# Kernel optimization log

Hardware: AMD Instinct MI355X
Metric: run time of the kernel (lower is better)

## Reference

```python
import jax, jax.numpy as jnp
import numpy as np

B, S, E, H = 4, 1024, 2048, 16
D = E // H  # head_dim = 128


def setup_inputs() -> dict:
    key = jax.random.key(0)
    k1, k2, k3, k4, k5 = jax.random.split(key, 5)
    scale = 1.0 / np.sqrt(E)
    return {
        "query": jax.random.normal(k1, (B, S, E), dtype=jnp.float32),
        "in_proj_weight": jax.random.normal(k2, (3 * E, E), dtype=jnp.float32) * scale,
        "in_proj_bias": jax.random.normal(k3, (3 * E,), dtype=jnp.float32) * 0.02,
        "out_proj_weight": jax.random.normal(k4, (E, E), dtype=jnp.float32) * scale,
        "out_proj_bias": jax.random.normal(k5, (E,), dtype=jnp.float32) * 0.02,
    }


def reference(query, in_proj_weight, in_proj_bias, out_proj_weight, out_proj_bias):
    b, s, e = query.shape
    d = e // H
    # fused QKV projection: [B,S,3E]
    proj = jnp.einsum("bse,fe->bsf", query, in_proj_weight) + in_proj_bias
    q, k, v = jnp.split(proj, 3, axis=-1)
    # [B,S,E] -> [B,H,S,D]
    def to_heads(t):
        return t.reshape(b, s, H, d).transpose(0, 2, 1, 3)
    q, k, v = to_heads(q), to_heads(k), to_heads(v)
    # scaled dot-product attention (non-causal, no mask, no dropout)
    scores = jnp.einsum("bhqd,bhkd->bhqk", q, k) / jnp.sqrt(jnp.asarray(d, q.dtype))
    attn = jax.nn.softmax(scores, axis=-1)
    ctx = jnp.einsum("bhqk,bhkd->bhqd", attn, v)
    # [B,H,S,D] -> [B,S,E]
    ctx = ctx.transpose(0, 2, 1, 3).reshape(b, s, e)
    out = jnp.einsum("bse,fe->bsf", ctx, out_proj_weight) + out_proj_bias
    return out
```

## Files before the change

### kernel.cpp

```cpp
#include <hip/hip_runtime.h>
#include <hip/hip_fp16.h>

#define F16 _Float16
typedef F16 f16x8 __attribute__((ext_vector_type(8)));
typedef F16 f16x4 __attribute__((ext_vector_type(4)));
typedef float f32x4 __attribute__((ext_vector_type(4)));

__global__ void cvt_f32_f16(const float* __restrict__ src, F16* __restrict__ dst, int n) {
    int idx = blockIdx.x * blockDim.x + threadIdx.x;
    int stride = gridDim.x * blockDim.x;
    for (int i = idx * 4; i < n; i += stride * 4) {
        float4 v = *reinterpret_cast<const float4*>(src + i);
        f16x4 o;
        o[0] = (F16)v.x; o[1] = (F16)v.y; o[2] = (F16)v.z; o[3] = (F16)v.w;
        *reinterpret_cast<f16x4*>(dst + i) = o;
    }
}

__device__ __forceinline__ void gl_lds16(const F16* g, F16* l) {
    __builtin_amdgcn_global_load_lds(
        (const __attribute__((address_space(1))) void*)g,
        (__attribute__((address_space(3))) void*)l, 16, 0, 0);
}

__global__ __launch_bounds__(512, 2) void gemm8qkv(
    const F16* __restrict__ A, const F16* __restrict__ Bw, const float* __restrict__ bias,
    F16* __restrict__ q_ws, F16* __restrict__ k_ws, F16* __restrict__ v_ws,
    int M, int N, int K)
{
    __shared__ __align__(16) F16 lds[2][4][8192];
    const int tid = threadIdx.x;
    const int w = tid >> 6, l = tid & 63;
    const int lr = l & 15, lg = l >> 4;
    const int wm = w >> 2, wn = w & 3;

    const int xcd = (int)blockIdx.x & 7, s5 = (int)blockIdx.x >> 3;
    const int mb = (xcd & 1) * 8 + s5 / 6;
    const int nb = (xcd >> 1) * 6 + s5 % 6;
    const long brow = (long)mb * 256, bcol = (long)nb * 256;

    const F16* rb0 = A + brow * K;
    const F16* rb1 = rb0 + 128 * (long)K;
    const F16* rb2 = Bw + bcol * K;
    const F16* rb3 = rb2 + 128 * (long)K;

    const int sr0 = ((tid >> 7) << 4) + (tid & 15);
    const int skk = (((tid >> 6) & 1) << 5) + (((tid >> 4) & 3) << 3);
    const int wb8 = (w << 6) * 8;

#define GISSUE(BUF, R, S, KT, RB) \
    gl_lds16(RB + (long)(sr0 + S * 64) * K + (KT) * 64 + skk, \
             &lds[BUF][R][S * 4096 + wb8])

    const int NK = K >> 6;

    f32x4 acc[8][4];
#pragma unroll
    for (int f = 0; f < 8; ++f)
#pragma unroll
        for (int nf = 0; nf < 4; ++nf) acc[f][nf] = f32x4{0.f, 0.f, 0.f, 0.f};

    GISSUE(0, 0, 0, 0, rb0); GISSUE(0, 0, 1, 0, rb0);
    GISSUE(0, 1, 0, 0, rb1); GISSUE(0, 1, 1, 0, rb1);
    GISSUE(0, 2, 0, 0, rb2); GISSUE(0, 2, 1, 0, rb2);
    GISSUE(0, 3, 0, 0, rb3); GISSUE(0, 3, 1, 0, rb3);
    if (NK > 1) {
        GISSUE(1, 2, 0, 1, rb2); GISSUE(1, 2, 1, 1, rb2);
        GISSUE(1, 3, 0, 1, rb3); GISSUE(1, 3, 1, 1, rb3);
        GISSUE(1, 0, 0, 1, rb0); GISSUE(1, 1, 0, 1, rb1);
        asm volatile("s_waitcnt vmcnt(6)" ::: "memory");
    } else {
        asm volatile("s_waitcnt vmcnt(0)" ::: "memory");
    }
    __builtin_amdgcn_s_barrier();

    for (int kt = 0; kt < NK; ++kt) {
        const int cur = kt & 1, nxt = cur ^ 1;
        const F16* Areg = &lds[cur][wm][0];
        const F16* Breg = &lds[cur][2 + (wn >> 1)][0];
        f16x8 b[4][2];
#pragma unroll
        for (int nf = 0; nf < 4; ++nf)
#pragma unroll
            for (int ks = 0; ks < 2; ++ks)
                b[nf][ks] = *reinterpret_cast<const f16x8*>(
                    Breg + ((((wn & 1) * 4 + nf) * 2 + ks) * 64 + l) * 8);
#pragma unroll
        for (int p = 0; p < 4; ++p) {
            f16x8 a[2][2];
#pragma unroll
            for (int mf = 0; mf < 2; ++mf)
#pragma unroll
                for (int ks = 0; ks < 2; ++ks)
                    a[mf][ks] = *reinterpret_cast<const f16x8*>(
                        Areg + (((2 * p + mf) * 2 + ks) * 64 + l) * 8);
            if (p == 0) {
                if (kt + 1 < NK) { GISSUE(nxt, 0, 1, kt + 1, rb0); GISSUE(nxt, 1, 1, kt + 1, rb1); }
            } else if (p == 1) {
                if (kt + 2 < NK) { GISSUE(cur, 2, 0, kt + 2, rb2); GISSUE(cur, 2, 1, kt + 2, rb2); }
            } else if (p == 2) {
                if (kt + 2 < NK) { GISSUE(cur, 3, 0, kt + 2, rb3); GISSUE(cur, 3, 1, kt + 2, rb3); }
            } else {
                if (kt + 2 < NK) { GISSUE(cur, 0, 0, kt + 2, rb0); GISSUE(cur, 1, 0, kt + 2, rb1); }
            }
            __builtin_amdgcn_sched_barrier(0);
            __builtin_amdgcn_s_barrier();
            asm volatile("s_waitcnt lgkmcnt(0)" ::: "memory");
            __builtin_amdgcn_sched_barrier(0);
            __builtin_amdgcn_s_setprio(1);
#pragma unroll
            for (int mf = 0; mf < 2; ++mf)
#pragma unroll
                for (int nf = 0; nf < 4; ++nf)
#pragma unroll
                    for (int ks = 0; ks < 2; ++ks)
                        acc[2 * p + mf][nf] = __builtin_amdgcn_mfma_f32_16x16x32_f16(
                            a[mf][ks], b[nf][ks], acc[2 * p + mf][nf], 0, 0, 0);
            __builtin_amdgcn_s_setprio(0);
            __builtin_amdgcn_sched_barrier(0);
            if (p == 3) {
                if (kt + 2 < NK) asm volatile("s_waitcnt vmcnt(6)" ::: "memory");
                else             asm volatile("s_waitcnt vmcnt(0)" ::: "memory");
            }
            __builtin_amdgcn_s_barrier();
        }
    }
#undef GISSUE

    const int col0 = (int)bcol + wn * 64;
    const int row0 = (int)brow + wm * 128;
    const int part = (int)(bcol >> 11);
    const int bI = row0 >> 10;
    const int sb = row0 & 1023;
    const float scl = (part == 0) ? 0.08838834764831845f : 1.0f;
#pragma unroll
    for (int nf = 0; nf < 4; ++nf) {
        const int gcol = col0 + nf * 16 + lr;
        const float bv = bias[gcol];
        const int d = gcol & 127;
        const int hh = (gcol >> 7) & 15;
        if (part == 2) {
            F16* dst0 = v_ws + ((long)((bI * 16 + hh) * 128 + d)) * 1024;
#pragma unroll
            for (int f = 0; f < 8; ++f) {
                f16x4 pv;
#pragma unroll
                for (int r = 0; r < 4; ++r) pv[r] = (F16)(acc[f][nf][r] + bv);
                *reinterpret_cast<f16x4*>(dst0 + sb + f * 16 + lg * 4) = pv;
            }
        } else {
            F16* dst0 = ((part == 0) ? q_ws : k_ws) + ((long)(bI * 16 + hh) * 1024) * 128 + d;
#pragma unroll
            for (int f = 0; f < 8; ++f)
#pragma unroll
                for (int r = 0; r < 4; ++r)
                    dst0[(long)(sb + f * 16 + lg * 4 + r) * 128] =
                        (F16)((acc[f][nf][r] + bv) * scl);
        }
    }
}

__global__ __launch_bounds__(512, 2) void gemm8out(
    const F16* __restrict__ A, const F16* __restrict__ Bw, const float* __restrict__ bias,
    float* __restrict__ fout, int M, int N, int K)
{
    __shared__ __align__(16) F16 lds[2][3][8192];
    const int tid = threadIdx.x;
    const int w = tid >> 6, l = tid & 63;
    const int lr = l & 15, lg = l >> 4;
    const int wm = w >> 2, wn = w & 3;

    const int xcd = (int)blockIdx.x & 7, s5 = (int)blockIdx.x >> 3;
    const int mb = (xcd & 3) * 8 + (s5 >> 2);
    const int nb = (xcd >> 2) * 4 + (s5 & 3);
    const long brow = (long)mb * 128, bcol = (long)nb * 256;

    const F16* rbA = A + brow * K;
    const F16* rb2 = Bw + bcol * K;
    const F16* rb3 = rb2 + 128 * (long)K;

    const int sr0 = ((tid >> 7) << 4) + (tid & 15);
    const int skk = (((tid >> 6) & 1) << 5) + (((tid >> 4) & 3) << 3);
    const int wb8 = (w << 6) * 8;

#define GISSUE(BUF, R, S, KT, RB) \
    gl_lds16(RB + (long)(sr0 + S * 64) * K + (KT) * 64 + skk, \
             &lds[BUF][R][S * 4096 + wb8])

    const int NK = K >> 6;

    f32x4 acc[4][4];
#pragma unroll
    for (int f = 0; f < 4; ++f)
#pragma unroll
        for (int nf = 0; nf < 4; ++nf) acc[f][nf] = f32x4{0.f, 0.f, 0.f, 0.f};

    GISSUE(0, 0, 0, 0, rbA); GISSUE(0, 0, 1, 0, rbA);
    GISSUE(0, 1, 0, 0, rb2); GISSUE(0, 1, 1, 0, rb2);
    GISSUE(0, 2, 0, 0, rb3); GISSUE(0, 2, 1, 0, rb3);
    if (NK > 1) {
        GISSUE(1, 1, 0, 1, rb2); GISSUE(1, 1, 1, 1, rb2);
        GISSUE(1, 2, 0, 1, rb3); GISSUE(1, 2, 1, 1, rb3);
        asm volatile("s_waitcnt vmcnt(4)" ::: "memory");
    } else {
        asm volatile("s_waitcnt vmcnt(0)" ::: "memory");
    }
    __builtin_amdgcn_s_barrier();

    for (int kt = 0; kt < NK; ++kt) {
        const int cur = kt & 1, nxt = cur ^ 1;
        const F16* Areg = &lds[cur][0][0];
        const F16* Breg = &lds[cur][1 + (wn >> 1)][0];
        f16x8 b[4][2];
#pragma unroll
        for (int nf = 0; nf < 4; ++nf)
#pragma unroll
            for (int ks = 0; ks < 2; ++ks)
                b[nf][ks] = *reinterpret_cast<const f16x8*>(
                    Breg + ((((wn & 1) * 4 + nf) * 2 + ks) * 64 + l) * 8);
#pragma unroll
        for (int p = 0; p < 2; ++p) {
            f16x8 a[2][2];
#pragma unroll
            for (int mf = 0; mf < 2; ++mf)
#pragma unroll
                for (int ks = 0; ks < 2; ++ks)
                    a[mf][ks] = *reinterpret_cast<const f16x8*>(
                        Areg + (((wm * 4 + 2 * p + mf) * 2 + ks) * 64 + l) * 8);
            if (p == 0) {
                if (kt + 1 < NK) { GISSUE(nxt, 0, 0, kt + 1, rbA); GISSUE(nxt, 0, 1, kt + 1, rbA); }
            } else {
                if (kt + 2 < NK) {
                    GISSUE(cur, 1, 0, kt + 2, rb2); GISSUE(cur, 1, 1, kt + 2, rb2);
                    GISSUE(cur, 2, 0, kt + 2, rb3); GISSUE(cur, 2, 1, kt + 2, rb3);
                }
            }
            __builtin_amdgcn_sched_barrier(0);
            __builtin_amdgcn_s_barrier();
            asm volatile("s_waitcnt lgkmcnt(0)" ::: "memory");
            __builtin_amdgcn_sched_barrier(0);
            __builtin_amdgcn_s_setprio(1);
#pragma unroll
            for (int mf = 0; mf < 2; ++mf)
#pragma unroll
                for (int nf = 0; nf < 4; ++nf)
#pragma unroll
                    for (int ks = 0; ks < 2; ++ks)
                        acc[2 * p + mf][nf] = __builtin_amdgcn_mfma_f32_16x16x32_f16(
                            a[mf][ks], b[nf][ks], acc[2 * p + mf][nf], 0, 0, 0);
            __builtin_amdgcn_s_setprio(0);
            __builtin_amdgcn_sched_barrier(0);
            if (p == 1) {
                if (kt + 2 < NK) asm volatile("s_waitcnt vmcnt(4)" ::: "memory");
                else             asm volatile("s_waitcnt vmcnt(0)" ::: "memory");
            }
            __builtin_amdgcn_s_barrier();
        }
    }
#undef GISSUE

    const int col0 = (int)bcol + wn * 64;
    const int row0 = (int)brow + wm * 64;
#pragma unroll
    for (int nf = 0; nf < 4; ++nf) {
        const int gcol = col0 + nf * 16 + lr;
        const float bv = bias[gcol];
#pragma unroll
        for (int f = 0; f < 4; ++f)
#pragma unroll
            for (int r = 0; r < 4; ++r)
                fout[(long)(row0 + f * 16 + lg * 4 + r) * N + gcol] = acc[f][nf][r] + bv;
    }
}

__global__ __launch_bounds__(256, 2) void attn_kernel(
    const F16* __restrict__ q_ws, const F16* __restrict__ k_ws,
    const F16* __restrict__ v_ws, F16* __restrict__ ctx)
{
    __shared__ __align__(16) F16 kt[2][64 * 128];
    __shared__ __align__(16) F16 vt[2][128 * 64];
    __shared__ __align__(16) F16 p_lds[4][2048];
    const int tid = threadIdx.x;
    const int w = tid >> 6, l = tid & 63;
    const int lr = l & 15, lg = l >> 4;
    const int work = (blockIdx.x & 7) * 64 + (blockIdx.x >> 3);
    const int bh = work >> 3, qt = work & 7;
    const int b = bh >> 4, h = bh & 15;
    const int q0 = qt * 128 + w * 32;

    const F16* kbh = k_ws + (long)bh * 1024 * 128;
    const F16* vbh = v_ws + (long)bh * 128 * 1024;

    f16x8 qf[2][4];
#pragma unroll
    for (int mi = 0; mi < 2; ++mi)
#pragma unroll
        for (int ks = 0; ks < 4; ++ks)
            qf[mi][ks] = *reinterpret_cast<const f16x8*>(
                q_ws + ((long)bh * 1024 + q0 + mi * 16 + lr) * 128 + ks * 32 + lg * 8);

    auto stage = [&](int buf, int kv0) {
#pragma unroll
        for (int t = 0; t < 4; ++t) {
            const int chunk = t * 256 + tid;
            const int row = chunk >> 4;
            const int colb = (chunk & 15) << 4;
            const int gcol = colb ^ ((row & 7) << 4);
            gl_lds16(kbh + (long)(kv0 + row) * 128 + (gcol >> 1),
                     &kt[buf][(t * 256 + w * 64) * 8]);
        }
#pragma unroll
        for (int t = 0; t < 4; ++t) {
            const int chunk = t * 256 + tid;
            const int d = chunk >> 3;
            const int colb = (chunk & 7) << 4;
            const int gcol = colb ^ ((d & 7) << 4);
            gl_lds16(vbh + (long)d * 1024 + kv0 + (gcol >> 1),
                     &vt[buf][(t * 256 + w * 64) * 8]);
        }
    };

    float mrun[2][4], lsum[2][4];
#pragma unroll
    for (int mi = 0; mi < 2; ++mi)
#pragma unroll
        for (int r = 0; r < 4; ++r) { mrun[mi][r] = -1e30f; lsum[mi][r] = 0.f; }
    f32x4 acc[2][8];
#pragma unroll
    for (int mi = 0; mi < 2; ++mi)
#pragma unroll
        for (int nf = 0; nf < 8; ++nf) acc[mi][nf] = f32x4{0.f, 0.f, 0.f, 0.f};

    stage(0, 0);
    __syncthreads();
    int cur = 0;
    for (int it = 0; it < 16; ++it) {
        if (it + 1 < 16) stage(cur ^ 1, (it + 1) * 64);

        f32x4 sc[2][4];
#pragma unroll
        for (int mi = 0; mi < 2; ++mi)
#pragma unroll
            for (int cf = 0; cf < 4; ++cf) sc[mi][cf] = f32x4{0.f, 0.f, 0.f, 0.f};
#pragma unroll
        for (int cf = 0; cf < 4; ++cf) {
#pragma unroll
            for (int ks = 0; ks < 4; ++ks) {
                const int row = cf * 16 + lr;
                const int eff = (ks * 64 + lg * 16) ^ ((row & 7) << 4);
                f16x8 kf = *reinterpret_cast<const f16x8*>(&kt[cur][row * 128 + (eff >> 1)]);
#pragma unroll
                for (int mi = 0; mi < 2; ++mi)
                    sc[mi][cf] = __builtin_amdgcn_mfma_f32_16x16x32_f16(qf[mi][ks], kf, sc[mi][cf], 0, 0, 0);
            }
        }

#pragma unroll
        for (int mi = 0; mi < 2; ++mi) {
            float t4[4];
#pragma unroll
            for (int r = 0; r < 4; ++r)
                t4[r] = fmaxf(fmaxf(sc[mi][0][r], sc[mi][1][r]), fmaxf(sc[mi][2][r], sc[mi][3][r]));
#pragma unroll
            for (int msk = 1; msk < 16; msk <<= 1)
#pragma unroll
                for (int r = 0; r < 4; ++r) t4[r] = fmaxf(t4[r], __shfl_xor(t4[r], msk));
            float al[4], rs[4], p[4][4];
#pragma unroll
            for (int r = 0; r < 4; ++r) {
                const float mn = fmaxf(mrun[mi][r], t4[r]);
                al[r] = __expf(mrun[mi][r] - mn);
                mrun[mi][r] = mn;
#pragma unroll
                for (int cf = 0; cf < 4; ++cf) p[cf][r] = __expf(sc[mi][cf][r] - mn);
                rs[r] = (p[0][r] + p[1][r]) + (p[2][r] + p[3][r]);
            }
#pragma unroll
            for (int msk = 1; msk < 16; msk <<= 1)
#pragma unroll
                for (int r = 0; r < 4; ++r) rs[r] += __shfl_xor(rs[r], msk);
#pragma unroll
            for (int r = 0; r < 4; ++r) lsum[mi][r] = lsum[mi][r] * al[r] + rs[r];
#pragma unroll
            for (int nf = 0; nf < 8; ++nf)
#pragma unroll
                for (int r = 0; r < 4; ++r) acc[mi][nf][r] *= al[r];
#pragma unroll
            for (int cf = 0; cf < 4; ++cf)
#pragma unroll
                for (int r = 0; r < 4; ++r) {
                    const int chunk = (mi * 2 + (cf >> 1)) * 64 + (lg * 4 + r) + ((cf & 1) * 2 + (lr >> 3)) * 16;
                    p_lds[w][chunk * 8 + (lr & 7)] = (F16)p[cf][r];
                }
        }

        f16x8 pf[2][2];
#pragma unroll
        for (int mi = 0; mi < 2; ++mi)
#pragma unroll
            for (int half = 0; half < 2; ++half)
                pf[mi][half] = *reinterpret_cast<const f16x8*>(&p_lds[w][((mi * 2 + half) * 64 + l) * 8]);
#pragma unroll
        for (int nf = 0; nf < 8; ++nf) {
#pragma unroll
            for (int half = 0; half < 2; ++half) {
                const int d = nf * 16 + lr;
                const int eff = (half * 64 + lg * 16) ^ ((d & 7) << 4);
                f16x8 vf = *reinterpret_cast<const f16x8*>(&vt[cur][d * 64 + (eff >> 1)]);
#pragma unroll
                for (int mi = 0; mi < 2; ++mi)
                    acc[mi][nf] = __builtin_amdgcn_mfma_f32_16x16x32_f16(pf[mi][half], vf, acc[mi][nf], 0, 0, 0);
            }
        }
        __syncthreads();
        cur ^= 1;
    }

#pragma unroll
    for (int mi = 0; mi < 2; ++mi) {
        float inv[4];
#pragma unroll
        for (int r = 0; r < 4; ++r) inv[r] = 1.f / lsum[mi][r];
#pragma unroll
        for (int nf = 0; nf < 8; ++nf)
#pragma unroll
            for (int r = 0; r < 4; ++r) {
                const int s = q0 + mi * 16 + lg * 4 + r;
                const int e = h * 128 + nf * 16 + lr;
                ctx[((long)(b * 1024 + s)) * 2048 + e] = (F16)(acc[mi][nf][r] * inv[r]);
            }
    }
}

extern "C" void kernel_launch(void* const* d_in, const int* in_sizes, int n_in,
                              void* d_out, int out_size, void* d_ws, size_t ws_size,
                              hipStream_t stream) {
    const float* query = (const float*)d_in[0];
    const float* w_in  = (const float*)d_in[1];
    const float* b_in  = (const float*)d_in[2];
    const float* w_out = (const float*)d_in[3];
    const float* b_out = (const float*)d_in[4];
    float* out = (float*)d_out;

    char* ws = (char*)d_ws;
    size_t off = 0;
    auto carve = [&](size_t bytes) -> void* {
        void* p = ws + off;
        off += (bytes + 255) & ~(size_t)255;
        return p;
    };
    F16* xq  = (F16*)carve(8388608ULL * 2);
    F16* wih = (F16*)carve(12582912ULL * 2);
    F16* woh = (F16*)carve(4194304ULL * 2);
    F16* qws = (F16*)carve(8388608ULL * 2);
    F16* kws = (F16*)carve(8388608ULL * 2);
    F16* vws = (F16*)carve(8388608ULL * 2);
    F16* ctx = (F16*)carve(8388608ULL * 2);

    cvt_f32_f16<<<1024, 256, 0, stream>>>(query, xq, 8388608);
    cvt_f32_f16<<<1024, 256, 0, stream>>>(w_in, wih, 12582912);
    cvt_f32_f16<<<512, 256, 0, stream>>>(w_out, woh, 4194304);

    gemm8qkv<<<384, 512, 0, stream>>>(xq, wih, b_in, qws, kws, vws, 4096, 6144, 2048);
    attn_kernel<<<512, 256, 0, stream>>>(qws, kws, vws, ctx);
    gemm8out<<<256, 512, 0, stream>>>(ctx, woh, b_out, out, 4096, 2048, 2048);
}
```

Measured before the change: 402.8 us.

## Transpose attention MFMA operands and add lazy softmax rescaling

Swaps the MFMA A/B operands in both QK^T and PV so each lane holds one query row. Row max and sum then need only two cross-lane shuffles instead of four, and P is written to LDS as swizzled f16x4 vectors. A wave-uniform threshold skips updating the running max and rescaling the accumulator when the new max exceeds the old by no more than 8. That trades a bounded exp growth in fp32 for fewer multiplies. The output store becomes vectorized f16x4 per row.

```diff
diff --git a/kernel.cpp b/kernel.cpp
--- a/kernel.cpp
+++ b/kernel.cpp
@@ -279,7 +279,7 @@
 {
     __shared__ __align__(16) F16 kt[2][64 * 128];
     __shared__ __align__(16) F16 vt[2][128 * 64];
-    __shared__ __align__(16) F16 p_lds[4][2048];
+    __shared__ __align__(16) F16 plds[4][2][1024];
     const int tid = threadIdx.x;
     const int w = tid >> 6, l = tid & 63;
     const int lr = l & 15, lg = l >> 4;
@@ -287,6 +287,7 @@
     const int bh = work >> 3, qt = work & 7;
     const int b = bh >> 4, h = bh & 15;
     const int q0 = qt * 128 + w * 32;
+    const int sw = (lr & 7) << 4;
 
     const F16* kbh = k_ws + (long)bh * 1024 * 128;
     const F16* vbh = v_ws + (long)bh * 128 * 1024;
@@ -320,11 +321,9 @@
         }
     };
 
-    float mrun[2][4], lsum[2][4];
-#pragma unroll
-    for (int mi = 0; mi < 2; ++mi)
-#pragma unroll
-        for (int r = 0; r < 4; ++r) { mrun[mi][r] = -1e30f; lsum[mi][r] = 0.f; }
+    float mrun[2], lsum[2];
+    mrun[0] = mrun[1] = -1e30f;
+    lsum[0] = lsum[1] = 0.f;
     f32x4 acc[2][8];
 #pragma unroll
     for (int mi = 0; mi < 2; ++mi)
@@ -351,65 +350,64 @@
                 f16x8 kf = *reinterpret_cast<const f16x8*>(&kt[cur][row * 128 + (eff >> 1)]);
 #pragma unroll
                 for (int mi = 0; mi < 2; ++mi)
-                    sc[mi][cf] = __builtin_amdgcn_mfma_f32_16x16x32_f16(qf[mi][ks], kf, sc[mi][cf], 0, 0, 0);
+                    sc[mi][cf] = __builtin_amdgcn_mfma_f32_16x16x32_f16(kf, qf[mi][ks], sc[mi][cf], 0, 0, 0);
             }
         }
 
 #pragma unroll
         for (int mi = 0; mi < 2; ++mi) {
-            float t4[4];
-#pragma unroll
-            for (int r = 0; r < 4; ++r)
-                t4[r] = fmaxf(fmaxf(sc[mi][0][r], sc[mi][1][r]), fmaxf(sc[mi][2][r], sc[mi][3][r]));
-#pragma unroll
-            for (int msk = 1; msk < 16; msk <<= 1)
-#pragma unroll
-                for (int r = 0; r < 4; ++r) t4[r] = fmaxf(t4[r], __shfl_xor(t4[r], msk));
-            float al[4], rs[4], p[4][4];
-#pragma unroll
-            for (int r = 0; r < 4; ++r) {
-                const float mn = fmaxf(mrun[mi][r], t4[r]);
-                al[r] = __expf(mrun[mi][r] - mn);
-                mrun[mi][r] = mn;
-#pragma unroll
-                for (int cf = 0; cf < 4; ++cf) p[cf][r] = __expf(sc[mi][cf][r] - mn);
-                rs[r] = (p[0][r] + p[1][r]) + (p[2][r] + p[3][r]);
-            }
-#pragma unroll
-            for (int msk = 1; msk < 16; msk <<= 1)
-#pragma unroll
-                for (int r = 0; r < 4; ++r) rs[r] += __shfl_xor(rs[r], msk);
-#pragma unroll
-            for (int r = 0; r < 4; ++r) lsum[mi][r] = lsum[mi][r] * al[r] + rs[r];
-#pragma unroll
-            for (int nf = 0; nf < 8; ++nf)
-#pragma unroll
-                for (int r = 0; r < 4; ++r) acc[mi][nf][r] *= al[r];
+            float nm = sc[mi][0][0];
 #pragma unroll
             for (int cf = 0; cf < 4; ++cf)
 #pragma unroll
+                for (int r = 0; r < 4; ++r) nm = fmaxf(nm, sc[mi][cf][r]);
+            nm = fmaxf(nm, __shfl_xor(nm, 16));
+            nm = fmaxf(nm, __shfl_xor(nm, 32));
+            const bool skip = __all(nm <= mrun[mi] + 8.0f);
+            float mn, al;
+            if (skip) { mn = mrun[mi]; al = 1.0f; }
+            else      { mn = fmaxf(mrun[mi], nm); al = __expf(mrun[mi] - mn); mrun[mi] = mn; }
+            float rs = 0.f;
+            char* prow = reinterpret_cast<char*>(&plds[w][mi][0]) + lr * 128;
+#pragma unroll
+            for (int cf = 0; cf < 4; ++cf) {
+                f16x4 pv;
+#pragma unroll
                 for (int r = 0; r < 4; ++r) {
-                    const int chunk = (mi * 2 + (cf >> 1)) * 64 + (lg * 4 + r) + ((cf & 1) * 2 + (lr >> 3)) * 16;
-                    p_lds[w][chunk * 8 + (lr & 7)] = (F16)p[cf][r];
+                    const float pe = __expf(sc[mi][cf][r] - mn);
+                    rs += pe;
+                    pv[r] = (F16)pe;
                 }
+                *reinterpret_cast<f16x4*>(prow + ((cf * 32 + lg * 8) ^ sw)) = pv;
+            }
+            rs += __shfl_xor(rs, 16);
+            rs += __shfl_xor(rs, 32);
+            lsum[mi] = lsum[mi] * al + rs;
+            if (!skip) {
+#pragma unroll
+                for (int nf = 0; nf < 8; ++nf)
+#pragma unroll
+                    for (int r = 0; r < 4; ++r) acc[mi][nf][r] *= al;
+            }
         }
 
         f16x8 pf[2][2];
 #pragma unroll
         for (int mi = 0; mi < 2; ++mi)
 #pragma unroll
-            for (int half = 0; half < 2; ++half)
-                pf[mi][half] = *reinterpret_cast<const f16x8*>(&p_lds[w][((mi * 2 + half) * 64 + l) * 8]);
+            for (int kvs = 0; kvs < 2; ++kvs)
+                pf[mi][kvs] = *reinterpret_cast<const f16x8*>(
+                    reinterpret_cast<char*>(&plds[w][mi][0]) + lr * 128 + ((kvs * 64 + lg * 16) ^ sw));
 #pragma unroll
         for (int nf = 0; nf < 8; ++nf) {
 #pragma unroll
-            for (int half = 0; half < 2; ++half) {
+            for (int kvs = 0; kvs < 2; ++kvs) {
                 const int d = nf * 16 + lr;
-                const int eff = (half * 64 + lg * 16) ^ ((d & 7) << 4);
+                const int eff = (kvs * 64 + lg * 16) ^ ((d & 7) << 4);
                 f16x8 vf = *reinterpret_cast<const f16x8*>(&vt[cur][d * 64 + (eff >> 1)]);
 #pragma unroll
                 for (int mi = 0; mi < 2; ++mi)
-                    acc[mi][nf] = __builtin_amdgcn_mfma_f32_16x16x32_f16(pf[mi][half], vf, acc[mi][nf], 0, 0, 0);
+                    acc[mi][nf] = __builtin_amdgcn_mfma_f32_16x16x32_f16(vf, pf[mi][kvs], acc[mi][nf], 0, 0, 0);
             }
         }
         __syncthreads();
@@ -418,17 +416,16 @@
 
 #pragma unroll
     for (int mi = 0; mi < 2; ++mi) {
-        float inv[4];
-#pragma unroll
-        for (int r = 0; r < 4; ++r) inv[r] = 1.f / lsum[mi][r];
-#pragma unroll
-        for (int nf = 0; nf < 8; ++nf)
-#pragma unroll
-            for (int r = 0; r < 4; ++r) {
-                const int s = q0 + mi * 16 + lg * 4 + r;
-                const int e = h * 128 + nf * 16 + lr;
-                ctx[((long)(b * 1024 + s)) * 2048 + e] = (F16)(acc[mi][nf][r] * inv[r]);
-            }
+        const float inv = 1.f / lsum[mi];
+        const int s = q0 + mi * 16 + lr;
+        F16* orow = ctx + ((long)(b * 1024 + s)) * 2048 + h * 128;
+#pragma unroll
+        for (int nf = 0; nf < 8; ++nf) {
+            f16x4 ov;
+#pragma unroll
+            for (int r = 0; r < 4; ++r) ov[r] = (F16)(acc[mi][nf][r] * inv);
+            *reinterpret_cast<f16x4*>(orow + nf * 16 + lg * 4) = ov;
+        }
     }
 }
 
```

After: 394.0 us. 1.02x faster.
